# Performance work log

Measured on AMD Instinct MI355X. Metric: run time of the kernel, lower is better.

The kernel has to match this reference:

```python
import jax, jax.numpy as jnp
import numpy as np

BN_EPS = 1e-5


def _tconv(X, w1, b1, w2, b2, w3, b3):
    # X: (B, T, N, C) -> conv over time with kernel (1, k), gated GLU-style
    Xp = X.transpose(0, 2, 1, 3)  # (B, N, T, C)
    def conv(w, b):
        return jax.lax.conv_general_dilated(
            Xp, w, (1, 1), 'VALID',
            dimension_numbers=('NHWC', 'HWIO', 'NHWC')) + b
    P = conv(w1, b1)
    Q = jax.nn.sigmoid(conv(w2, b2))
    R = conv(w3, b3)
    H = jax.nn.relu(P * Q + R)
    return H.transpose(0, 2, 1, 3)  # (B, T-k+1, N, Cout)


def _cheb(x, ei, W, b):
    # Batched ChebConv (sym norm, lambda_max=2 => L_hat = -D^-1/2 A D^-1/2)
    # x: (S, N, F), ei: (S, 2, E), W: (K, F, Fout)
    S, N, F = x.shape
    row, col = ei[:, 0], ei[:, 1]           # (S, E)
    ones = jnp.ones(ei.shape[-1], x.dtype)
    def norm_one(r, c):
        deg = jax.ops.segment_sum(ones, r, num_segments=N)
        dis = jnp.where(deg > 0, jax.lax.rsqrt(jnp.maximum(deg, 1.)), 0.)
        return -dis[r] * dis[c]
    w = jax.vmap(norm_one)(row, col)        # (S, E), constant wrt floats
    def prop(xs, r, c, ws):
        return jax.ops.segment_sum(ws[:, None] * xs[c], r, num_segments=N)
    propv = jax.vmap(prop)
    Tx = [x, propv(x, row, col, w)]
    for _ in range(W.shape[0] - 2):
        Tx.append(2. * propv(Tx[-1], row, col, w) - Tx[-2])
    return jnp.einsum('ksnf,kfo->sno', jnp.stack(Tx), W) + b


def _forward(X, tc1_w1, tc1_b1, tc1_w2, tc1_b2, tc1_w3, tc1_b3,
             cheb_w, cheb_b,
             tc2_w1, tc2_b1, tc2_w2, tc2_b2, tc2_w3, tc2_b3,
             bn_gamma, bn_beta, conv3_w, conv3_b, f1_w, f1_b, edge_index):
    T0 = _tconv(X, tc1_w1, tc1_b1, tc1_w2, tc1_b2, tc1_w3, tc1_b3)  # (B,38,N,H)
    B, Tt, N, H = T0.shape
    ei = edge_index[:, :Tt].reshape(B * Tt, 2, edge_index.shape[-1])
    G = _cheb(T0.reshape(B * Tt, N, H), ei, cheb_w, cheb_b)
    G = jax.nn.relu(G.reshape(B, Tt, N, H))
    T2 = _tconv(G, tc2_w1, tc2_b1, tc2_w2, tc2_b2, tc2_w3, tc2_b3)  # (B,36,N,Co)
    # BatchNorm2d over channel dim = num_nodes (training-mode batch stats)
    Tn = T2.transpose(0, 2, 1, 3)  # (B, N, T, C)
    mean = Tn.mean(axis=(0, 2, 3), keepdims=True)
    var = Tn.var(axis=(0, 2, 3), keepdims=True)
    Tn = (Tn - mean) * jax.lax.rsqrt(var + BN_EPS)
    Tn = Tn * bn_gamma[None, :, None, None] + bn_beta[None, :, None, None]
    Tb = Tn.transpose(0, 2, 1, 3)                 # (B, T, N, C)
    Tr = Tb.reshape(B, Tb.shape[1], -1)           # (B, T, N*C=3200)
    y = jax.lax.conv_general_dilated(
        Tr[:, None, :, :], conv3_w, (1, 1), 'VALID',
        dimension_numbers=('NCHW', 'OIHW', 'NCHW'))  # (B,128,T-2,1)
    y = y + conv3_b[None, :, None, None]
    y = y[:, :, :, 0]
    pooled = y.mean(axis=2)                        # AvgPool1d over full length
    return pooled @ f1_w + f1_b                    # (B, 3200)


def setup_inputs() -> dict:
    key = jax.random.key(0)
    ks = jax.random.split(key, 20)
    B, Tw, N, Cin, H, Co, E = 32, 40, 50, 2, 128, 64, 800
    KT, K = 3, 3
    s = 0.05
    d = {
        'X': jax.random.normal(ks[0], (B, Tw, N, Cin), jnp.float32),
        'edge_index': jax.random.randint(ks[1], (B, Tw, 2, E), 0, N),
        'tc1_w1': jax.random.normal(ks[2], (1, KT, Cin, H), jnp.float32) * s,
        'tc1_b1': jnp.zeros((H,), jnp.float32),
        'tc1_w2': jax.random.normal(ks[3], (1, KT, Cin, H), jnp.float32) * s,
        'tc1_b2': jnp.zeros((H,), jnp.float32),
        'tc1_w3': jax.random.normal(ks[4], (1, KT, Cin, H), jnp.float32) * s,
        'tc1_b3': jnp.zeros((H,), jnp.float32),
        'cheb_w': jax.random.normal(ks[5], (K, H, H), jnp.float32) * s,
        'cheb_b': jnp.zeros((H,), jnp.float32),
        'tc2_w1': jax.random.normal(ks[6], (1, KT, H, Co), jnp.float32) * s,
        'tc2_b1': jnp.zeros((Co,), jnp.float32),
        'tc2_w2': jax.random.normal(ks[7], (1, KT, H, Co), jnp.float32) * s,
        'tc2_b2': jnp.zeros((Co,), jnp.float32),
        'tc2_w3': jax.random.normal(ks[8], (1, KT, H, Co), jnp.float32) * s,
        'tc2_b3': jnp.zeros((Co,), jnp.float32),
        'bn_gamma': jnp.ones((N,), jnp.float32),
        'bn_beta': jnp.zeros((N,), jnp.float32),
        'conv3_w': jax.random.normal(ks[9], (128, 1, 3, N * Co), jnp.float32) * 0.01,
        'conv3_b': jnp.zeros((128,), jnp.float32),
        'f1_w': jax.random.normal(ks[10], (128, N * Co), jnp.float32) * s,
        'f1_b': jnp.zeros((N * Co,), jnp.float32),
    }
    return d


def reference(X, tc1_w1, tc1_b1, tc1_w2, tc1_b2, tc1_w3, tc1_b3,
              cheb_w, cheb_b,
              tc2_w1, tc2_b1, tc2_w2, tc2_b2, tc2_w3, tc2_b3,
              bn_gamma, bn_beta, conv3_w, conv3_b, f1_w, f1_b, edge_index):
    return _forward(X, tc1_w1, tc1_b1, tc1_w2, tc1_b2, tc1_w3, tc1_b3,
                    cheb_w, cheb_b,
                    tc2_w1, tc2_b1, tc2_w2, tc2_b2, tc2_w3, tc2_b3,
                    bn_gamma, bn_beta, conv3_w, conv3_b, f1_w, f1_b, edge_index)
```

## Files before the change

### kernel.cpp

```cpp
#include <hip/hip_runtime.h>
#include <hip/hip_bf16.h>

#define BB 32
#define TW 40
#define NN 50
#define HH 128
#define CO 64
#define EE 800
#define TT 38
#define TT2 36
#define TPOOL 34
#define NCO 3200
#define SS (BB*TT)
#define NPAD 64
#define RPAD (SS*NPAD)

#define PB_US ((size_t)RPAD * HH)
#define PB_BYTES (PB_US * 2)

typedef __attribute__((ext_vector_type(8))) short s16x8;
typedef __attribute__((ext_vector_type(16))) float f32x16;
typedef unsigned short us;

static __device__ __forceinline__ unsigned int f2bf_u(float x) {
    unsigned int u = __float_as_uint(x);
    return (u + 0x7fffu + ((u >> 16) & 1u)) >> 16;
}
static __device__ __forceinline__ float bfu2f(unsigned int h) {
    return __uint_as_float(h << 16);
}
static __device__ __forceinline__ size_t fragoff32(int m, int c) {
    return (size_t)(c >> 4) * 512 + ((c >> 3) & 1) * 256 + m * 8 + (c & 7);
}
#define MFMA(a, b, c) __builtin_amdgcn_mfma_f32_32x32x16_bf16((a), (b), (c), 0, 0, 0)

__global__ __launch_bounds__(256) void k_wprep(
    const float* __restrict__ cw,
    const float* __restrict__ tw1, const float* __restrict__ tw2, const float* __restrict__ tw3,
    us* __restrict__ VTh, us* __restrict__ VTl,
    us* __restrict__ WTh, us* __restrict__ WTl,
    float* __restrict__ pooled, float* __restrict__ gpart)
{
    int idx = blockIdx.x * 256 + threadIdx.x;
    float v; us *dh, *dl; int col, k;
    if (idx < 128 * 384) {
        col = idx / 384; k = idx % 384;
        if (k < 128)      v = cw[k * 128 + col] - cw[32768 + k * 128 + col];
        else if (k < 256) v = cw[16384 + (k - 128) * 128 + col];
        else              v = 2.f * cw[32768 + (k - 256) * 128 + col];
        dh = VTh; dl = VTl;
    } else if (idx < 128 * 384 + 192 * 384) {
        int i2 = idx - 128 * 384;
        col = i2 / 384; k = i2 % 384;
        int gg = col >> 6, o = col & 63;
        const float* src = (gg == 0) ? tw1 : (gg == 1) ? tw2 : tw3;
        v = src[k * 64 + o];
        dh = WTh; dl = WTl;
    } else {
        int z = idx - (128 * 384 + 192 * 384);
        if (z < 4096) pooled[z] = 0.f;
        else if (z < 4224) gpart[z - 4096] = 0.f;
        return;
    }
    size_t off = ((size_t)((col >> 5) * 24 + (k >> 4)) * 64 + ((k >> 3) & 1) * 32 + (col & 31)) * 8
               + (k & 7);
    unsigned int h = f2bf_u(v);
    dh[off] = (us)h;
    dl[off] = (us)f2bf_u(v - bfu2f(h));
}

#define TAS 136
#define TBS 72
#define LMS 53
__global__ __launch_bounds__(256) void k_cheb(
    const int* __restrict__ EI, const float* __restrict__ X,
    const float* __restrict__ w1, const float* __restrict__ b1,
    const float* __restrict__ w2, const float* __restrict__ b2,
    const float* __restrict__ w3, const float* __restrict__ b3,
    const us* __restrict__ VTh, const us* __restrict__ VTl,
    const float* __restrict__ bias,
    us* __restrict__ Gh)
{
    __shared__ __align__(16) char smem[61440];
    us* TbA = (us*)smem;
    us* TbB = (us*)(smem + 17408);
    us* Pa  = (us*)(smem + 35840);
    float* Lm = (float*)(smem + 35840);
    us* LA  = (us*)(smem + 53248);
    float* Xs = (float*)(smem + 53248);
    int* deg  = (int*)(smem + 53248 + 1216);
    float* dis = (float*)(smem + 53248 + 1216 + 224);

    int g = blockIdx.x;
    int tid = threadIdx.x;
    int b = g / TT, t = g % TT;
    const int* row = EI + (size_t)(b * TW + t) * 2 * EE;
    const int* col = row + EE;

    {
        s16x8 zz = {0, 0, 0, 0, 0, 0, 0, 0};
        for (int i = tid; i < 2240; i += 256) ((s16x8*)smem)[i] = zz;
    }
    for (int i = tid; i < 52 * LMS; i += 256) Lm[i] = 0.f;
    for (int i = tid; i < 300; i += 256) Xs[i] = X[(size_t)(b * TW + t) * 100 + i];
    if (tid < NN) deg[tid] = 0;
    __syncthreads();

    {
        int c = tid & 127, nh = tid >> 7;
        float wr1[6], wr2[6], wr3[6];
#pragma unroll
        for (int q = 0; q < 6; q++) {
            wr1[q] = w1[q * HH + c];
            wr2[q] = w2[q * HH + c];
            wr3[q] = w3[q * HH + c];
        }
        float bv1 = b1[c], bv2 = b2[c], bv3 = b3[c];
        for (int n = nh; n < NN; n += 2) {
            float P = bv1, Q = bv2, R = bv3;
#pragma unroll
            for (int q = 0; q < 6; q++) {
                float x = Xs[(q >> 1) * 100 + n * 2 + (q & 1)];
                P += x * wr1[q]; Q += x * wr2[q]; R += x * wr3[q];
            }
            float sg = 1.f / (1.f + expf(-Q));
            float v = P * sg + R;
            v = v > 0.f ? v : 0.f;
            us h = (us)f2bf_u(v);
            TbA[n * TAS + c] = h;
            TbB[c * TBS + n] = h;
        }
    }
    __syncthreads();
    for (int e = tid; e < EE; e += 256) atomicAdd(&deg[row[e]], 1);
    __syncthreads();
    if (tid < NN) dis[tid] = deg[tid] > 0 ? rsqrtf((float)deg[tid]) : 0.f;
    __syncthreads();
    for (int e = tid; e < EE; e += 256) {
        int r = row[e], cc = col[e];
        atomicAdd(&Lm[r * LMS + cc], -dis[r] * dis[cc]);
    }
    __syncthreads();
    for (int ent = tid; ent < 512; ent += 256) {
        int lanee = ent & 63;
        int ks = (ent >> 6) & 3;
        int mt = ent >> 8;
        int m = mt * 32 + (lanee & 31);
        int kb = ks * 16 + (lanee >> 5) * 8;
        s16x8 v;
#pragma unroll
        for (int j = 0; j < 8; j++) {
            int k = kb + j;
            float lv = (m < NN && k < NN) ? Lm[m * LMS + k] : 0.f;
            v[j] = (short)f2bf_u(lv);
        }
        *(s16x8*)(LA + ent * 8) = v;
    }
    __syncthreads();

    int lane = tid & 63;
    int w = tid >> 6;
    int rg = w >> 1, fh = w & 1;
    int nl = lane & 31;
    int khalf = lane >> 5;
    size_t laneoff = (size_t)lane * 8;

    const us* vh0 = VTh + (size_t)(fh * 2) * 12288 + laneoff;
    const us* vh1 = VTh + (size_t)(fh * 2 + 1) * 12288 + laneoff;
    const us* vl0 = VTl + (size_t)(fh * 2) * 12288 + laneoff;
    const us* vl1 = VTl + (size_t)(fh * 2 + 1) * 12288 + laneoff;

    int mrowA = rg * 32 + nl;
    int kbb = khalf * 8;

    f32x16 gacc0, gacc1, d0, d1;
#pragma unroll
    for (int r = 0; r < 16; r++) { gacc0[r] = 0.f; gacc1[r] = 0.f; d0[r] = 0.f; d1[r] = 0.f; }

#pragma unroll
    for (int ks = 0; ks < 4; ks++) {
        s16x8 afr = *(const s16x8*)(LA + ((rg * 4 + ks) * 64 + lane) * 8);
        int kb = ks * 16 + kbb;
        s16x8 bf0 = *(const s16x8*)(TbB + (fh * 64 + nl) * TBS + kb);
        s16x8 bf1 = *(const s16x8*)(TbB + (fh * 64 + 32 + nl) * TBS + kb);
        d0 = MFMA(afr, bf0, d0);
        d1 = MFMA(afr, bf1, d1);
    }
#pragma unroll
    for (int ks = 0; ks < 8; ks++) {
        s16x8 ah = *(const s16x8*)(TbA + mrowA * TAS + ks * 16 + kbb);
        s16x8 bh0 = *(const s16x8*)(vh0 + ks * 512);
        s16x8 bl0 = *(const s16x8*)(vl0 + ks * 512);
        s16x8 bh1 = *(const s16x8*)(vh1 + ks * 512);
        s16x8 bl1 = *(const s16x8*)(vl1 + ks * 512);
        gacc0 = MFMA(ah, bh0, gacc0); gacc0 = MFMA(ah, bl0, gacc0);
        gacc1 = MFMA(ah, bh1, gacc1); gacc1 = MFMA(ah, bl1, gacc1);
    }
    __syncthreads();
#pragma unroll
    for (int r = 0; r < 16; r++) {
        int mrow = (r & 3) + 8 * (r >> 2) + 4 * khalf;
        int node = rg * 32 + mrow;
        int f0 = fh * 64 + nl, f1 = f0 + 32;
        us h0 = (us)f2bf_u(d0[r]);
        us h1 = (us)f2bf_u(d1[r]);
        Pa[node * TAS + f0] = h0;
        Pa[node * TAS + f1] = h1;
        TbB[f0 * TBS + node] = h0;
        TbB[f1 * TBS + node] = h1;
    }
    __syncthreads();

#pragma unroll
    for (int r = 0; r < 16; r++) { d0[r] = 0.f; d1[r] = 0.f; }
#pragma unroll
    for (int ks = 0; ks < 4; ks++) {
        s16x8 afr = *(const s16x8*)(LA + ((rg * 4 + ks) * 64 + lane) * 8);
        int kb = ks * 16 + kbb;
        s16x8 bf0 = *(const s16x8*)(TbB + (fh * 64 + nl) * TBS + kb);
        s16x8 bf1 = *(const s16x8*)(TbB + (fh * 64 + 32 + nl) * TBS + kb);
        d0 = MFMA(afr, bf0, d0);
        d1 = MFMA(afr, bf1, d1);
    }
#pragma unroll
    for (int ks = 0; ks < 8; ks++) {
        s16x8 ah = *(const s16x8*)(Pa + mrowA * TAS + ks * 16 + kbb);
        s16x8 bh0 = *(const s16x8*)(vh0 + (8 + ks) * 512);
        s16x8 bl0 = *(const s16x8*)(vl0 + (8 + ks) * 512);
        s16x8 bh1 = *(const s16x8*)(vh1 + (8 + ks) * 512);
        s16x8 bl1 = *(const s16x8*)(vl1 + (8 + ks) * 512);
        gacc0 = MFMA(ah, bh0, gacc0); gacc0 = MFMA(ah, bl0, gacc0);
        gacc1 = MFMA(ah, bh1, gacc1); gacc1 = MFMA(ah, bl1, gacc1);
    }
    __syncthreads();
#pragma unroll
    for (int r = 0; r < 16; r++) {
        int mrow = (r & 3) + 8 * (r >> 2) + 4 * khalf;
        int node = rg * 32 + mrow;
        int f0 = fh * 64 + nl, f1 = f0 + 32;
        Pa[node * TAS + f0] = (us)f2bf_u(d0[r]);
        Pa[node * TAS + f1] = (us)f2bf_u(d1[r]);
    }
    __syncthreads();
#pragma unroll
    for (int ks = 0; ks < 8; ks++) {
        s16x8 ah = *(const s16x8*)(Pa + mrowA * TAS + ks * 16 + kbb);
        s16x8 bh0 = *(const s16x8*)(vh0 + (16 + ks) * 512);
        s16x8 bl0 = *(const s16x8*)(vl0 + (16 + ks) * 512);
        s16x8 bh1 = *(const s16x8*)(vh1 + (16 + ks) * 512);
        s16x8 bl1 = *(const s16x8*)(vl1 + (16 + ks) * 512);
        gacc0 = MFMA(ah, bh0, gacc0); gacc0 = MFMA(ah, bl0, gacc0);
        gacc1 = MFMA(ah, bh1, gacc1); gacc1 = MFMA(ah, bl1, gacc1);
    }

    int c0 = fh * 64 + nl, c1 = c0 + 32;
    float bv0 = bias[c0], bv1 = bias[c1];
    size_t gb = (size_t)g * 8192 + (size_t)rg * 4096;
#pragma unroll
    for (int r = 0; r < 16; r++) {
        int mrow = (r & 3) + 8 * (r >> 2) + 4 * khalf;
        float v0 = gacc0[r] + bv0; v0 = v0 > 0.f ? v0 : 0.f;
        float v1 = gacc1[r] + bv1; v1 = v1 > 0.f ? v1 : 0.f;
        Gh[gb + fragoff32(mrow, c0)] = (us)f2bf_u(v0);
        Gh[gb + fragoff32(mrow, c1)] = (us)f2bf_u(v1);
    }
}

__global__ __launch_bounds__(128) void k_tc2(
    const us* __restrict__ Gh,
    const us* __restrict__ WTh, const us* __restrict__ WTl,
    const float* __restrict__ tb1, const float* __restrict__ tb2, const float* __restrict__ tb3,
    float* __restrict__ T2, float* __restrict__ gpart)
{
    __shared__ float nsum[64], nss[64];
    int tid = threadIdx.x;
    int lane = tid & 63;
    int w = tid >> 6;
    int nl = lane & 31;
    size_t laneoff = (size_t)lane * 8;
    int bt36 = blockIdx.x;
    int b = bt36 / TT2, t = bt36 % TT2;
    if (tid < 64) { nsum[tid] = 0.f; nss[tid] = 0.f; }
    __syncthreads();

    const us* A0[3];
    const us* A1[3];
#pragma unroll
    for (int k3 = 0; k3 < 3; k3++) {
        size_t tb = (size_t)(b * TT + t + k3) * 8192;
        A0[k3] = Gh + tb + laneoff;
        A1[k3] = Gh + tb + 4096 + laneoff;
    }
    const us* Bh[3];
    const us* Bl[3];
#pragma unroll
    for (int g3 = 0; g3 < 3; g3++) {
        size_t cb = (size_t)(g3 * 2 + w) * 12288 + laneoff;
        Bh[g3] = WTh + cb;
        Bl[g3] = WTl + cb;
    }

    f32x16 aP0, aQ0, aR0, aP1, aQ1, aR1;
#pragma unroll
    for (int r = 0; r < 16; r++) {
        aP0[r] = 0.f; aQ0[r] = 0.f; aR0[r] = 0.f;
        aP1[r] = 0.f; aQ1[r] = 0.f; aR1[r] = 0.f;
    }

#pragma unroll
    for (int k3 = 0; k3 < 3; k3++) {
#pragma unroll
        for (int ls = 0; ls < 8; ls++) {
            int offB = (k3 * 8 + ls) * 512;
            s16x8 a0 = *(const s16x8*)(A0[k3] + ls * 512);
            s16x8 a1 = *(const s16x8*)(A1[k3] + ls * 512);
            s16x8 ph = *(const s16x8*)(Bh[0] + offB);
            s16x8 pl = *(const s16x8*)(Bl[0] + offB);
            s16x8 qh = *(const s16x8*)(Bh[1] + offB);
            s16x8 ql = *(const s16x8*)(Bl[1] + offB);
            s16x8 rh = *(const s16x8*)(Bh[2] + offB);
            s16x8 rl = *(const s16x8*)(Bl[2] + offB);
            aP0 = MFMA(a0, ph, aP0); aP0 = MFMA(a0, pl, aP0);
            aQ0 = MFMA(a0, qh, aQ0); aQ0 = MFMA(a0, ql, aQ0);
            aR0 = MFMA(a0, rh, aR0); aR0 = MFMA(a0, rl, aR0);
            aP1 = MFMA(a1, ph, aP1); aP1 = MFMA(a1, pl, aP1);
            aQ1 = MFMA(a1, qh, aQ1); aQ1 = MFMA(a1, ql, aQ1);
            aR1 = MFMA(a1, rh, aR1); aR1 = MFMA(a1, rl, aR1);
        }
    }

    int o = w * 32 + nl;
    float bP = tb1[o], bQ = tb2[o], bR = tb3[o];
    int rbase = (lane >> 5) * 4;
#pragma unroll
    for (int r = 0; r < 16; r++) {
        int m = (r & 3) + 8 * (r >> 2) + rbase;
        {
            float P = aP0[r] + bP, Q = aQ0[r] + bQ, R = aR0[r] + bR;
            float sg = 1.f / (1.f + expf(-Q));
            float v = P * sg + R;
            v = v > 0.f ? v : 0.f;
            T2[((size_t)bt36 * NN + m) * CO + o] = v;
            float sv = v, sq = v * v;
#pragma unroll
            for (int off = 16; off > 0; off >>= 1) {
                sv += __shfl_down(sv, off, 32);
                sq += __shfl_down(sq, off, 32);
            }
            if (nl == 0) { atomicAdd(&nsum[m], sv); atomicAdd(&nss[m], sq); }
        }
        int n1 = 32 + m;
        if (n1 < NN) {
            float P = aP1[r] + bP, Q = aQ1[r] + bQ, R = aR1[r] + bR;
            float sg = 1.f / (1.f + expf(-Q));
            float v = P * sg + R;
            v = v > 0.f ? v : 0.f;
            T2[((size_t)bt36 * NN + n1) * CO + o] = v;
            float sv = v, sq = v * v;
#pragma unroll
            for (int off = 16; off > 0; off >>= 1) {
                sv += __shfl_down(sv, off, 32);
                sq += __shfl_down(sq, off, 32);
            }
            if (nl == 0) { atomicAdd(&nsum[n1], sv); atomicAdd(&nss[n1], sq); }
        }
    }
    __syncthreads();
    if (tid < NN) {
        atomicAdd(&gpart[tid], nsum[tid]);
        atomicAdd(&gpart[64 + tid], nss[tid]);
    }
}

__global__ __launch_bounds__(64) void k_bnfin(const float* __restrict__ gpart, float* __restrict__ stats)
{
    int n = threadIdx.x;
    if (n < NN) {
        const float inv = 1.f / (float)(BB * TT2 * CO);
        float m = gpart[n] * inv;
        float var = gpart[64 + n] * inv - m * m;
        stats[n] = m;
        stats[64 + n] = rsqrtf(var + 1e-5f);
    }
}

__global__ __launch_bounds__(256) void k_upool(
    const float* __restrict__ T2, const float* __restrict__ stats,
    const float* __restrict__ gamma, const float* __restrict__ beta,
    const float* __restrict__ W3, float* __restrict__ pooled)
{
    __shared__ __align__(16) float Ul[48 * 36 + 32];
    __shared__ float Ws[128 * 9];
    int blk = blockIdx.x;
    int jc = blk * 16;
    int n0 = jc >> 6;
    int tid = threadIdx.x;
    float mn = stats[n0], is = stats[64 + n0];
    float sc = is * gamma[n0];
    float off = (float)TPOOL * beta[n0] - (float)TPOOL * mn * sc;

    {
        int j = tid & 15, b0 = tid >> 4;
#pragma unroll
        for (int bp = 0; bp < 2; bp++) {
            int bb = b0 + 16 * bp;
            const float* p = T2 + (size_t)bb * TT2 * NCO + jc + j;
            float s0 = 0.f;
            for (int t = 0; t < TPOOL; t++) s0 += p[(size_t)t * NCO];
            float s1 = s0 - p[0] + p[(size_t)34 * NCO];
            float s2 = s1 - p[(size_t)1 * NCO] + p[(size_t)35 * NCO];
            Ul[(0 * 16 + j) * 36 + bb] = s0 * sc + off;
            Ul[(1 * 16 + j) * 36 + bb] = s1 * sc + off;
            Ul[(2 * 16 + j) * 36 + bb] = s2 * sc + off;
        }
    }
    __syncthreads();

    int o = tid & 127, bq = tid >> 7;
    float acc[16];
#pragma unroll
    for (int i = 0; i < 16; i++) acc[i] = 0.f;

    for (int kjc = 0; kjc < 48; kjc += 8) {
        __syncthreads();
#pragma unroll
        for (int p4 = 0; p4 < 4; p4++) {
            int idx = p4 * 256 + tid;
            int oo = idx >> 3, q = idx & 7;
            int kj = kjc + q;
            Ws[oo * 9 + q] = W3[(size_t)oo * 9600 + (kj >> 4) * 3200 + jc + (kj & 15)];
        }
        __syncthreads();
#pragma unroll
        for (int q = 0; q < 8; q++) {
            float wv = Ws[o * 9 + q];
            const float* up = &Ul[(kjc + q) * 36 + bq * 16];
#pragma unroll
            for (int i4 = 0; i4 < 4; i4++) {
                float4 u = *(const float4*)(up + i4 * 4);
                acc[i4 * 4 + 0] += wv * u.x;
                acc[i4 * 4 + 1] += wv * u.y;
                acc[i4 * 4 + 2] += wv * u.z;
                acc[i4 * 4 + 3] += wv * u.w;
            }
        }
    }
#pragma unroll
    for (int i = 0; i < 16; i++)
        atomicAdd(&pooled[(size_t)(bq * 16 + i) * 128 + o], acc[i]);
}

__global__ __launch_bounds__(256) void k_final(
    const float* __restrict__ pooled, const float* __restrict__ b3c,
    const float* __restrict__ f1w, const float* __restrict__ f1b,
    float* __restrict__ out)
{
    int idx = blockIdx.x * 256 + threadIdx.x;
    if (idx >= BB * NCO) return;
    int q = idx % NCO;
    int b = idx / NCO;
    const float inv = 1.f / (float)TPOOL;
    float acc = f1b[q];
    const float* pp = pooled + b * 128;
    for (int o = 0; o < 128; o++) acc += (pp[o] * inv + b3c[o]) * f1w[(size_t)o * NCO + q];
    out[idx] = acc;
}

extern "C" void kernel_launch(void* const* d_in, const int* in_sizes, int n_in,
                              void* d_out, int out_size, void* d_ws, size_t ws_size,
                              hipStream_t stream)
{
    const float* X       = (const float*)d_in[0];
    const int*   EI      = (const int*)d_in[1];
    const float* tc1_w1  = (const float*)d_in[2];
    const float* tc1_b1  = (const float*)d_in[3];
    const float* tc1_w2  = (const float*)d_in[4];
    const float* tc1_b2  = (const float*)d_in[5];
    const float* tc1_w3  = (const float*)d_in[6];
    const float* tc1_b3  = (const float*)d_in[7];
    const float* cheb_w  = (const float*)d_in[8];
    const float* cheb_b  = (const float*)d_in[9];
    const float* tc2_w1  = (const float*)d_in[10];
    const float* tc2_b1  = (const float*)d_in[11];
    const float* tc2_w2  = (const float*)d_in[12];
    const float* tc2_b2  = (const float*)d_in[13];
    const float* tc2_w3  = (const float*)d_in[14];
    const float* tc2_b3  = (const float*)d_in[15];
    const float* bn_g    = (const float*)d_in[16];
    const float* bn_b    = (const float*)d_in[17];
    const float* conv3_w = (const float*)d_in[18];
    const float* conv3_b = (const float*)d_in[19];
    const float* f1_w    = (const float*)d_in[20];
    const float* f1_b    = (const float*)d_in[21];

    char* base = (char*)d_ws;
    us*    Gh     = (us*)base;
    float* T2     = (float*)(base + PB_BYTES);
    float* pooled = (float*)(base + PB_BYTES + 14745600);
    float* stats  = (float*)(base + PB_BYTES + 14761984);
    float* gpart  = (float*)(base + PB_BYTES + 14762496);
    us*    VTh    = (us*)(base + PB_BYTES + 14763008);
    us*    VTl    = VTh + 49152;
    us*    WTh    = VTl + 49152;
    us*    WTl    = WTh + 73728;

    k_wprep<<<497, 256, 0, stream>>>(cheb_w, tc2_w1, tc2_w2, tc2_w3, VTh, VTl, WTh, WTl, pooled, gpart);
    k_cheb<<<SS, 256, 0, stream>>>(EI, X, tc1_w1, tc1_b1, tc1_w2, tc1_b2, tc1_w3, tc1_b3,
                                   VTh, VTl, cheb_b, Gh);
    k_tc2<<<BB * TT2, 128, 0, stream>>>(Gh, WTh, WTl, tc2_b1, tc2_b2, tc2_b3, T2, gpart);
    k_bnfin<<<1, 64, 0, stream>>>(gpart, stats);
    k_upool<<<200, 256, 0, stream>>>(T2, stats, bn_g, bn_b, conv3_w, pooled);
    k_final<<<(BB * NCO + 255) / 256, 256, 0, stream>>>(pooled, conv3_b, f1_w, f1_b, (float*)d_out);
}
```

Baseline: 249.2 us.

## Split tc2 into node tiles, store T2 in bf16, separate BN stats pass, retile final GEMV

The tc2 kernel now launches two blocks per (b,t), one per 32-node tile, using an XCD-aware block swizzle. It writes its output as bf16 instead of fp32, which halves T2 traffic, and drops the in-kernel atomic BN statistics. A new k_bnpart kernel computes per-node partial sums from the bf16 T2, and k_bnfin reduces those partials. k_final stages the pooled vectors in shared memory so that each block covers 8 output columns for all batches, which improves reuse of the f1_w reads. Storing T2 in bf16 before BN and pooling adds rounding error, and the extra stats kernel re-reads T2.

```diff
diff --git a/kernel.cpp b/kernel.cpp
--- a/kernel.cpp
+++ b/kernel.cpp
@@ -39,7 +39,7 @@
     const float* __restrict__ tw1, const float* __restrict__ tw2, const float* __restrict__ tw3,
     us* __restrict__ VTh, us* __restrict__ VTl,
     us* __restrict__ WTh, us* __restrict__ WTl,
-    float* __restrict__ pooled, float* __restrict__ gpart)
+    float* __restrict__ pooled)
 {
     int idx = blockIdx.x * 256 + threadIdx.x;
     float v; us *dh, *dl; int col, k;
@@ -59,7 +59,6 @@
     } else {
         int z = idx - (128 * 384 + 192 * 384);
         if (z < 4096) pooled[z] = 0.f;
-        else if (z < 4224) gpart[z - 4096] = 0.f;
         return;
     }
     size_t off = ((size_t)((col >> 5) * 24 + (k >> 4)) * 64 + ((k >> 3) & 1) * 32 + (col & 31)) * 8
@@ -270,27 +269,22 @@
     const us* __restrict__ Gh,
     const us* __restrict__ WTh, const us* __restrict__ WTl,
     const float* __restrict__ tb1, const float* __restrict__ tb2, const float* __restrict__ tb3,
-    float* __restrict__ T2, float* __restrict__ gpart)
-{
-    __shared__ float nsum[64], nss[64];
+    us* __restrict__ T2)
+{
     int tid = threadIdx.x;
     int lane = tid & 63;
     int w = tid >> 6;
     int nl = lane & 31;
     size_t laneoff = (size_t)lane * 8;
-    int bt36 = blockIdx.x;
+    int i = blockIdx.x;
+    int vb = (i & 7) * 288 + (i >> 3);
+    int bt36 = vb >> 1, ntile = vb & 1;
     int b = bt36 / TT2, t = bt36 % TT2;
-    if (tid < 64) { nsum[tid] = 0.f; nss[tid] = 0.f; }
-    __syncthreads();
-
-    const us* A0[3];
-    const us* A1[3];
-#pragma unroll
-    for (int k3 = 0; k3 < 3; k3++) {
-        size_t tb = (size_t)(b * TT + t + k3) * 8192;
-        A0[k3] = Gh + tb + laneoff;
-        A1[k3] = Gh + tb + 4096 + laneoff;
-    }
+
+    const us* A[3];
+#pragma unroll
+    for (int k3 = 0; k3 < 3; k3++)
+        A[k3] = Gh + (size_t)(b * TT + t + k3) * 8192 + (size_t)ntile * 4096 + laneoff;
     const us* Bh[3];
     const us* Bl[3];
 #pragma unroll
@@ -300,32 +294,25 @@
         Bl[g3] = WTl + cb;
     }
 
-    f32x16 aP0, aQ0, aR0, aP1, aQ1, aR1;
-#pragma unroll
-    for (int r = 0; r < 16; r++) {
-        aP0[r] = 0.f; aQ0[r] = 0.f; aR0[r] = 0.f;
-        aP1[r] = 0.f; aQ1[r] = 0.f; aR1[r] = 0.f;
-    }
+    f32x16 aP, aQ, aR;
+#pragma unroll
+    for (int r = 0; r < 16; r++) { aP[r] = 0.f; aQ[r] = 0.f; aR[r] = 0.f; }
 
 #pragma unroll
     for (int k3 = 0; k3 < 3; k3++) {
 #pragma unroll
         for (int ls = 0; ls < 8; ls++) {
             int offB = (k3 * 8 + ls) * 512;
-            s16x8 a0 = *(const s16x8*)(A0[k3] + ls * 512);
-            s16x8 a1 = *(const s16x8*)(A1[k3] + ls * 512);
+            s16x8 a0 = *(const s16x8*)(A[k3] + ls * 512);
             s16x8 ph = *(const s16x8*)(Bh[0] + offB);
             s16x8 pl = *(const s16x8*)(Bl[0] + offB);
             s16x8 qh = *(const s16x8*)(Bh[1] + offB);
             s16x8 ql = *(const s16x8*)(Bl[1] + offB);
             s16x8 rh = *(const s16x8*)(Bh[2] + offB);
             s16x8 rl = *(const s16x8*)(Bl[2] + offB);
-            aP0 = MFMA(a0, ph, aP0); aP0 = MFMA(a0, pl, aP0);
-            aQ0 = MFMA(a0, qh, aQ0); aQ0 = MFMA(a0, ql, aQ0);
-            aR0 = MFMA(a0, rh, aR0); aR0 = MFMA(a0, rl, aR0);
-            aP1 = MFMA(a1, ph, aP1); aP1 = MFMA(a1, pl, aP1);
-            aQ1 = MFMA(a1, qh, aQ1); aQ1 = MFMA(a1, ql, aQ1);
-            aR1 = MFMA(a1, rh, aR1); aR1 = MFMA(a1, rl, aR1);
+            aP = MFMA(a0, ph, aP); aP = MFMA(a0, pl, aP);
+            aQ = MFMA(a0, qh, aQ); aQ = MFMA(a0, ql, aQ);
+            aR = MFMA(a0, rh, aR); aR = MFMA(a0, rl, aR);
         }
     }
 
@@ -335,57 +322,55 @@
 #pragma unroll
     for (int r = 0; r < 16; r++) {
         int m = (r & 3) + 8 * (r >> 2) + rbase;
-        {
-            float P = aP0[r] + bP, Q = aQ0[r] + bQ, R = aR0[r] + bR;
+        int node = ntile * 32 + m;
+        if (node < NN) {
+            float P = aP[r] + bP, Q = aQ[r] + bQ, R = aR[r] + bR;
             float sg = 1.f / (1.f + expf(-Q));
             float v = P * sg + R;
             v = v > 0.f ? v : 0.f;
-            T2[((size_t)bt36 * NN + m) * CO + o] = v;
-            float sv = v, sq = v * v;
-#pragma unroll
-            for (int off = 16; off > 0; off >>= 1) {
-                sv += __shfl_down(sv, off, 32);
-                sq += __shfl_down(sq, off, 32);
-            }
-            if (nl == 0) { atomicAdd(&nsum[m], sv); atomicAdd(&nss[m], sq); }
-        }
-        int n1 = 32 + m;
-        if (n1 < NN) {
-            float P = aP1[r] + bP, Q = aQ1[r] + bQ, R = aR1[r] + bR;
-            float sg = 1.f / (1.f + expf(-Q));
-            float v = P * sg + R;
-            v = v > 0.f ? v : 0.f;
-            T2[((size_t)bt36 * NN + n1) * CO + o] = v;
-            float sv = v, sq = v * v;
-#pragma unroll
-            for (int off = 16; off > 0; off >>= 1) {
-                sv += __shfl_down(sv, off, 32);
-                sq += __shfl_down(sq, off, 32);
-            }
-            if (nl == 0) { atomicAdd(&nsum[n1], sv); atomicAdd(&nss[n1], sq); }
-        }
-    }
-    __syncthreads();
-    if (tid < NN) {
-        atomicAdd(&gpart[tid], nsum[tid]);
-        atomicAdd(&gpart[64 + tid], nss[tid]);
-    }
-}
-
-__global__ __launch_bounds__(64) void k_bnfin(const float* __restrict__ gpart, float* __restrict__ stats)
+            T2[((size_t)bt36 * NN + node) * CO + o] = (us)f2bf_u(v);
+        }
+    }
+}
+
+__global__ __launch_bounds__(256) void k_bnpart(const us* __restrict__ T2, float* __restrict__ partial)
+{
+    int n = blockIdx.x >> 3, c = blockIdx.x & 7;
+    int tid = threadIdx.x;
+    float s = 0.f, ss = 0.f;
+    for (int i = tid; i < 144 * 64; i += 256) {
+        int bt = c * 144 + (i >> 6), o = i & 63;
+        float v = bfu2f(T2[((size_t)bt * NN + n) * CO + o]);
+        s += v; ss += v * v;
+    }
+    for (int off = 32; off > 0; off >>= 1) { s += __shfl_down(s, off, 64); ss += __shfl_down(ss, off, 64); }
+    __shared__ float rs[4], rss[4];
+    int lane = tid & 63, wv = tid >> 6;
+    if (lane == 0) { rs[wv] = s; rss[wv] = ss; }
+    __syncthreads();
+    if (tid == 0) {
+        partial[n * 8 + c] = rs[0] + rs[1] + rs[2] + rs[3];
+        partial[400 + n * 8 + c] = rss[0] + rss[1] + rss[2] + rss[3];
+    }
+}
+
+__global__ __launch_bounds__(64) void k_bnfin(const float* __restrict__ partial, float* __restrict__ stats)
 {
     int n = threadIdx.x;
     if (n < NN) {
+        float s = 0.f, ss = 0.f;
+#pragma unroll
+        for (int c = 0; c < 8; c++) { s += partial[n * 8 + c]; ss += partial[400 + n * 8 + c]; }
         const float inv = 1.f / (float)(BB * TT2 * CO);
-        float m = gpart[n] * inv;
-        float var = gpart[64 + n] * inv - m * m;
+        float m = s * inv;
+        float var = ss * inv - m * m;
         stats[n] = m;
         stats[64 + n] = rsqrtf(var + 1e-5f);
     }
 }
 
 __global__ __launch_bounds__(256) void k_upool(
-    const float* __restrict__ T2, const float* __restrict__ stats,
+    const us* __restrict__ T2, const float* __restrict__ stats,
     const float* __restrict__ gamma, const float* __restrict__ beta,
     const float* __restrict__ W3, float* __restrict__ pooled)
 {
@@ -404,11 +389,11 @@
 #pragma unroll
         for (int bp = 0; bp < 2; bp++) {
             int bb = b0 + 16 * bp;
-            const float* p = T2 + (size_t)bb * TT2 * NCO + jc + j;
+            const us* p = T2 + (size_t)bb * TT2 * NCO + jc + j;
             float s0 = 0.f;
-            for (int t = 0; t < TPOOL; t++) s0 += p[(size_t)t * NCO];
-            float s1 = s0 - p[0] + p[(size_t)34 * NCO];
-            float s2 = s1 - p[(size_t)1 * NCO] + p[(size_t)35 * NCO];
+            for (int t = 0; t < TPOOL; t++) s0 += bfu2f(p[(size_t)t * NCO]);
+            float s1 = s0 - bfu2f(p[0]) + bfu2f(p[(size_t)34 * NCO]);
+            float s2 = s1 - bfu2f(p[(size_t)1 * NCO]) + bfu2f(p[(size_t)35 * NCO]);
             Ul[(0 * 16 + j) * 36 + bb] = s0 * sc + off;
             Ul[(1 * 16 + j) * 36 + bb] = s1 * sc + off;
             Ul[(2 * 16 + j) * 36 + bb] = s2 * sc + off;
@@ -455,15 +440,22 @@
     const float* __restrict__ f1w, const float* __restrict__ f1b,
     float* __restrict__ out)
 {
-    int idx = blockIdx.x * 256 + threadIdx.x;
-    if (idx >= BB * NCO) return;
-    int q = idx % NCO;
-    int b = idx / NCO;
+    __shared__ float pb[32 * 129];
+    int tid = threadIdx.x;
     const float inv = 1.f / (float)TPOOL;
+    for (int i = tid; i < 4096; i += 256) {
+        int b = i >> 7, o = i & 127;
+        pb[b * 129 + o] = pooled[b * 128 + o] * inv + b3c[o];
+    }
+    __syncthreads();
+    int q = blockIdx.x * 8 + (tid & 7);
+    int b = tid >> 3;
     float acc = f1b[q];
-    const float* pp = pooled + b * 128;
-    for (int o = 0; o < 128; o++) acc += (pp[o] * inv + b3c[o]) * f1w[(size_t)o * NCO + q];
-    out[idx] = acc;
+    const float* wq = f1w + q;
+    const float* pbb = pb + b * 129;
+#pragma unroll 4
+    for (int o = 0; o < 128; o++) acc += pbb[o] * wq[(size_t)o * NCO];
+    out[(size_t)b * NCO + q] = acc;
 }
 
 extern "C" void kernel_launch(void* const* d_in, const int* in_sizes, int n_in,
@@ -495,20 +487,21 @@
 
     char* base = (char*)d_ws;
     us*    Gh     = (us*)base;
-    float* T2     = (float*)(base + PB_BYTES);
-    float* pooled = (float*)(base + PB_BYTES + 14745600);
-    float* stats  = (float*)(base + PB_BYTES + 14761984);
-    float* gpart  = (float*)(base + PB_BYTES + 14762496);
-    us*    VTh    = (us*)(base + PB_BYTES + 14763008);
+    us*    T2     = (us*)(base + PB_BYTES);
+    float* pooled = (float*)(base + PB_BYTES + 7372800);
+    float* stats  = (float*)(base + PB_BYTES + 7389184);
+    float* partial= (float*)(base + PB_BYTES + 7389696);
+    us*    VTh    = (us*)(base + PB_BYTES + 7392896);
     us*    VTl    = VTh + 49152;
     us*    WTh    = VTl + 49152;
     us*    WTl    = WTh + 73728;
 
-    k_wprep<<<497, 256, 0, stream>>>(cheb_w, tc2_w1, tc2_w2, tc2_w3, VTh, VTl, WTh, WTl, pooled, gpart);
+    k_wprep<<<496, 256, 0, stream>>>(cheb_w, tc2_w1, tc2_w2, tc2_w3, VTh, VTl, WTh, WTl, pooled);
     k_cheb<<<SS, 256, 0, stream>>>(EI, X, tc1_w1, tc1_b1, tc1_w2, tc1_b2, tc1_w3, tc1_b3,
                                    VTh, VTl, cheb_b, Gh);
-    k_tc2<<<BB * TT2, 128, 0, stream>>>(Gh, WTh, WTl, tc2_b1, tc2_b2, tc2_b3, T2, gpart);
-    k_bnfin<<<1, 64, 0, stream>>>(gpart, stats);
+    k_tc2<<<2304, 128, 0, stream>>>(Gh, WTh, WTl, tc2_b1, tc2_b2, tc2_b3, T2);
+    k_bnpart<<<NN * 8, 256, 0, stream>>>(T2, partial);
+    k_bnfin<<<1, 64, 0, stream>>>(partial, stats);
     k_upool<<<200, 256, 0, stream>>>(T2, stats, bn_g, bn_b, conv3_w, pooled);
-    k_final<<<(BB * NCO + 255) / 256, 256, 0, stream>>>(pooled, conv3_b, f1_w, f1_b, (float*)d_out);
-}
+    k_final<<<NCO / 8, 256, 0, stream>>>(pooled, conv3_b, f1_w, f1_b, (float*)d_out);
+}
```

After: 234.6 us. -5.9%, faster.
